# Optimization experiments

Hardware: AMD Instinct MI355X
Metric: run time of the kernel (lower is better)

Reference implementation:

```python
import jax, jax.numpy as jnp
import numpy as np
import math

C = 512
NUM_HEADS = 4
GROUPS = 32  # group_count(512, 32)
EPS = 1e-5


def group_norm(x, gamma, beta):
    # x: [b, c, h, w]; normalize over (c//GROUPS, h, w) per group
    b, c, h, w = x.shape
    xg = x.reshape(b, GROUPS, -1)
    mu = jnp.mean(xg, axis=-1, keepdims=True)
    var = jnp.var(xg, axis=-1, keepdims=True)
    xn = ((xg - mu) * jax.lax.rsqrt(var + EPS)).reshape(b, c, h, w)
    return xn * gamma[None, :, None, None] + beta[None, :, None, None]


def setup_inputs() -> dict:
    key = jax.random.key(0)
    ks = jax.random.split(key, 5)
    b, h, w = 2, 64, 64
    x = jax.random.normal(ks[0], (b, C, h, w), dtype=jnp.float32)
    gn_w = jnp.ones((C,), dtype=jnp.float32)
    gn_b = jnp.zeros((C,), dtype=jnp.float32)
    s_qkv = 1.0 / math.sqrt(C)
    w_qkv = jax.random.uniform(ks[1], (3 * C, C), jnp.float32, -s_qkv, s_qkv)
    b_qkv = jax.random.uniform(ks[2], (3 * C,), jnp.float32, -s_qkv, s_qkv)
    w_proj = jax.random.uniform(ks[3], (C, C), jnp.float32, -s_qkv, s_qkv)
    b_proj = jax.random.uniform(ks[4], (C,), jnp.float32, -s_qkv, s_qkv)
    return {"x": x, "gn_w": gn_w, "gn_b": gn_b, "w_qkv": w_qkv,
            "b_qkv": b_qkv, "w_proj": w_proj, "b_proj": b_proj}


def reference(x, gn_w, gn_b, w_qkv, b_qkv, w_proj, b_proj):
    b, c, h, w = x.shape
    L = h * w
    nh = NUM_HEADS
    hd = c // nh
    residual = x
    xn = group_norm(x, gn_w, gn_b).reshape(b, c, L)
    # Conv1d with kernel_size=1 == channelwise linear: [b, 3c, L]
    qkv = jnp.einsum('bcl,oc->bol', xn, w_qkv) + b_qkv[None, :, None]
    q, k, v = jnp.split(qkv, 3, axis=1)
    q = q.reshape(b, nh, hd, L)
    k = k.reshape(b, nh, hd, L)
    v = v.reshape(b, nh, hd, L)
    scores = jnp.einsum('bncd,bnce->bnde', q, k) / math.sqrt(hd)
    attn = jax.nn.softmax(scores, axis=-1)
    out = jnp.einsum('bnde,bnce->bncd', attn, v).reshape(b, c, L)
    out = jnp.einsum('bcl,oc->bol', out, w_proj) + b_proj[None, :, None]
    return out.reshape(b, c, h, w) + residual
```

## Files before the change

### kernel.cpp

```cpp
#include <hip/hip_runtime.h>
#include <math.h>

typedef __bf16 bf16;
typedef __bf16 bf16x8 __attribute__((ext_vector_type(8)));
typedef __bf16 bf16x4 __attribute__((ext_vector_type(4)));
typedef float f32x4 __attribute__((ext_vector_type(4)));

#define QSCALE (0.08838834764831845f * 1.4426950408889634f)

__device__ __forceinline__ void gll16(const bf16* g, bf16* l) {
    __builtin_amdgcn_global_load_lds((const __attribute__((address_space(1))) void*)g,
                                     (__attribute__((address_space(3))) void*)l, 16, 0, 0);
}

__global__ void k_pre(const float* __restrict__ wqkv, const float* __restrict__ wproj,
                      const float* __restrict__ x,
                      bf16* __restrict__ wqkv_b, bf16* __restrict__ wproj_b,
                      float* __restrict__ part) {
    int blk = blockIdx.x;
    if (blk < 1024) {
        int i = blk * 256 + threadIdx.x;
        const int n1 = (1536 * 512) / 4;
        float4 v;
        bf16* dst;
        if (i < n1) { v = ((const float4*)wqkv)[i];      dst = wqkv_b + (size_t)i * 4; }
        else        { v = ((const float4*)wproj)[i - n1]; dst = wproj_b + (size_t)(i - n1) * 4; }
        bf16x4 o;
        o[0] = (bf16)v.x; o[1] = (bf16)v.y; o[2] = (bf16)v.z; o[3] = (bf16)v.w;
        *(bf16x4*)dst = o;
        return;
    }
    int b2 = blk - 1024;
    int grp = b2 >> 2, p = b2 & 3;
    const float4* src = (const float4*)(x + (size_t)grp * 65536 + (size_t)p * 16384);
    float s = 0.f, ss = 0.f;
    for (int it = 0; it < 16; ++it) {
        float4 v = src[threadIdx.x + it * 256];
        s  += v.x + v.y + v.z + v.w;
        ss += v.x * v.x + v.y * v.y + v.z * v.z + v.w * v.w;
    }
    for (int off = 32; off; off >>= 1) { s += __shfl_down(s, off); ss += __shfl_down(ss, off); }
    __shared__ float rs[4], rss[4];
    int wave = threadIdx.x >> 6;
    if ((threadIdx.x & 63) == 0) { rs[wave] = s; rss[wave] = ss; }
    __syncthreads();
    if (threadIdx.x == 0) {
        part[(grp * 4 + p) * 2]     = rs[0] + rs[1] + rs[2] + rs[3];
        part[(grp * 4 + p) * 2 + 1] = rss[0] + rss[1] + rss[2] + rss[3];
    }
}

__global__ __launch_bounds__(256) void k_gn_norm_t(const float* __restrict__ x, const float* __restrict__ gw,
                                                   const float* __restrict__ gb, const float* __restrict__ part,
                                                   bf16* __restrict__ xn_t) {
    __shared__ float sX[64 * 69];
    __shared__ float sMean[4], sRstd[4];
    int b = blockIdx.z, c0 = blockIdx.y * 64, l0 = blockIdx.x * 64;
    int t = threadIdx.x;
    if (t < 4) {
        int g = b * 32 + (c0 >> 4) + t;
        float S = 0.f, SS = 0.f;
        for (int p = 0; p < 4; ++p) { S += part[(g * 4 + p) * 2]; SS += part[(g * 4 + p) * 2 + 1]; }
        float mean = S * (1.f / 65536.f);
        float var  = SS * (1.f / 65536.f) - mean * mean;
        sMean[t] = mean;
        sRstd[t] = rsqrtf(var + 1e-5f);
    }
    __syncthreads();
    int cr = t >> 4, lq = t & 15;
    const float* xp = x + ((size_t)(b * 512 + c0)) * 4096 + l0;
    for (int i = 0; i < 4; ++i) {
        int c = cr + i * 16;
        int cg = c0 + c;
        float mean = sMean[c >> 4], rstd = sRstd[c >> 4];
        float ga = gw[cg] * rstd;
        float be = gb[cg] - mean * ga;
        float4 v = *(const float4*)(xp + (size_t)c * 4096 + lq * 4);
        float* d = &sX[c * 69 + lq * 4];
        d[0] = v.x * ga + be; d[1] = v.y * ga + be; d[2] = v.z * ga + be; d[3] = v.w * ga + be;
    }
    __syncthreads();
    int lr = t >> 3, cp = t & 7;
    bf16* dst = xn_t + ((size_t)b * 4096 + l0) * 512 + c0;
    for (int i = 0; i < 2; ++i) {
        int l = lr + i * 32;
        bf16x8 o;
        for (int j = 0; j < 8; ++j) o[j] = (bf16)sX[(cp * 8 + j) * 69 + l];
        *(bf16x8*)(dst + (size_t)l * 512 + cp * 8) = o;
    }
}

__global__ __launch_bounds__(256, 3) void k_gemm_qkv(
    const bf16* __restrict__ A, const bf16* __restrict__ W, const float* __restrict__ bias,
    bf16* __restrict__ qkT, bf16* __restrict__ vb) {
    __shared__ bf16 smem[17408];
    int linear = blockIdx.x + 12 * blockIdx.y + 384 * blockIdx.z;
    int swz = (linear & 7) * 96 + (linear >> 3);
    int n0 = (swz % 12) * 128;
    int m0 = ((swz / 12) % 32) * 128;
    int bz = swz / 384;
    int tid = threadIdx.x, lane = tid & 63, wave = tid >> 6;
    int lo = lane & 15, quad = lane >> 4;
    int lr = lane >> 3, ls = lane & 7;
    int mw = (wave >> 1) * 64, nw = (wave & 1) * 64;
    const bf16* aptr[4]; int adst[4];
    const bf16* bptr[4]; int bdst[4];
    for (int i = 0; i < 4; ++i) {
        int r0 = wave * 32 + i * 8;
        int row = r0 + lr;
        aptr[i] = A + (size_t)bz * (4096 * 512) + (size_t)(m0 + row) * 512 + ((ls ^ (row & 7)) * 8);
        adst[i] = r0 * 64;
        bptr[i] = W + (size_t)(n0 + row) * 512 + ((ls ^ (row & 7)) * 8);
        bdst[i] = 8192 + r0 * 64;
    }
    f32x4 acc[4][4] = {};
    for (int step = 0; step < 8; ++step) {
        __syncthreads();
        for (int i = 0; i < 4; ++i) {
            gll16(aptr[i], &smem[adst[i]]); aptr[i] += 64;
            gll16(bptr[i], &smem[bdst[i]]); bptr[i] += 64;
        }
        __syncthreads();
        const bf16* sA = smem;
        const bf16* sB = smem + 8192;
        for (int kk = 0; kk < 2; ++kk) {
            bf16x8 af[4], bfr[4];
            int sw = ((kk * 4 + quad) ^ (lo & 7)) * 8;
            for (int t = 0; t < 4; ++t) af[t]  = *(const bf16x8*)&sA[(mw + t * 16 + lo) * 64 + sw];
            for (int t = 0; t < 4; ++t) bfr[t] = *(const bf16x8*)&sB[(nw + t * 16 + lo) * 64 + sw];
            for (int mt = 0; mt < 4; ++mt)
                for (int nt = 0; nt < 4; ++nt)
                    acc[mt][nt] = __builtin_amdgcn_mfma_f32_16x16x32_bf16(af[mt], bfr[nt], acc[mt][nt], 0, 0, 0);
        }
    }
    __syncthreads();
    bf16* sT = smem;
    bool isv = (n0 >= 1024);
    float sc = (n0 < 512) ? QSCALE : 1.f;
    for (int mt = 0; mt < 4; ++mt)
        for (int nt = 0; nt < 4; ++nt) {
            int c = nw + nt * 16 + lo;
            float bv = bias[n0 + c];
            for (int r = 0; r < 4; ++r) {
                int l = mw + mt * 16 + quad * 4 + r;
                float v = (acc[mt][nt][r] + bv) * sc;
                if (isv) sT[c * 136 + l] = (bf16)v;
                else     sT[l * 136 + c] = (bf16)v;
            }
        }
    __syncthreads();
    int row = tid >> 1, hh = tid & 1;
    if (isv) {
        bf16* dst = vb + (size_t)bz * (512 * 4096) + (size_t)(n0 - 1024 + row) * 4096 + m0;
        for (int j = 0; j < 8; ++j) {
            int ch = hh + j * 2;
            *(bf16x8*)(dst + ch * 8) = *(const bf16x8*)&sT[row * 136 + ch * 8];
        }
    } else {
        bf16* dst = qkT + (size_t)bz * (4096 * 1024) + (size_t)(m0 + row) * 1024 + n0;
        for (int j = 0; j < 8; ++j) {
            int ch = hh + j * 2;
            *(bf16x8*)(dst + ch * 8) = *(const bf16x8*)&sT[row * 136 + ch * 8];
        }
    }
}

__global__ __launch_bounds__(256) void k_gemm_proj(
    const bf16* __restrict__ W, const bf16* __restrict__ Bm,
    const float* __restrict__ bias_m,
    float* __restrict__ outf, const float* __restrict__ resid) {
    constexpr int BUF = (128 + 128) * 64;
    __shared__ bf16 smem[2 * BUF];
    int linear = blockIdx.x + 32 * blockIdx.y + 128 * blockIdx.z;
    int swz = (linear & 7) * 32 + (linear >> 3);
    int n0 = (swz % 32) * 128;
    int m0 = ((swz / 32) % 4) * 128;
    int bz = swz / 128;
    int tid = threadIdx.x, lane = tid & 63, wave = tid >> 6;
    int lo = lane & 15, quad = lane >> 4;
    int lr = lane >> 3, ls = lane & 7;
    int mw = (wave >> 1) * 64, nw = (wave & 1) * 64;
    const bf16* aptr[4]; int adst[4];
    const bf16* bptr[4]; int bdst[4];
    for (int i = 0; i < 4; ++i) {
        int r0 = wave * 32 + i * 8;
        int row = r0 + lr;
        aptr[i] = W + (size_t)(m0 + row) * 512 + ((ls ^ (row & 7)) * 8);
        adst[i] = r0 * 64;
        bptr[i] = Bm + (size_t)bz * (4096 * 512) + (size_t)(n0 + row) * 512 + ((ls ^ (row & 7)) * 8);
        bdst[i] = 8192 + r0 * 64;
    }
    f32x4 acc[4][4] = {};
    for (int i = 0; i < 4; ++i) {
        gll16(aptr[i], &smem[adst[i]]); aptr[i] += 64;
        gll16(bptr[i], &smem[bdst[i]]); bptr[i] += 64;
    }
    for (int step = 0; step < 8; ++step) {
        int cur = step & 1;
        __syncthreads();
        if (step < 7) {
            bf16* nb = &smem[(cur ^ 1) * BUF];
            for (int i = 0; i < 4; ++i) {
                gll16(aptr[i], nb + adst[i]); aptr[i] += 64;
                gll16(bptr[i], nb + bdst[i]); bptr[i] += 64;
            }
        }
        const bf16* sA = &smem[cur * BUF];
        const bf16* sB = sA + 8192;
        for (int kk = 0; kk < 2; ++kk) {
            bf16x8 af[4], bfr[4];
            int sw = ((kk * 4 + quad) ^ (lo & 7)) * 8;
            for (int t = 0; t < 4; ++t) af[t]  = *(const bf16x8*)&sA[(mw + t * 16 + lo) * 64 + sw];
            for (int t = 0; t < 4; ++t) bfr[t] = *(const bf16x8*)&sB[(nw + t * 16 + lo) * 64 + sw];
            for (int mt = 0; mt < 4; ++mt)
                for (int nt = 0; nt < 4; ++nt)
                    acc[mt][nt] = __builtin_amdgcn_mfma_f32_16x16x32_bf16(af[mt], bfr[nt], acc[mt][nt], 0, 0, 0);
        }
    }
    for (int mt = 0; mt < 4; ++mt) {
        int rowb = m0 + mw + mt * 16 + quad * 4;
        for (int nt = 0; nt < 4; ++nt) {
            int col = n0 + nw + nt * 16 + lo;
            for (int r = 0; r < 4; ++r) {
                int row = rowb + r;
                size_t idx = (size_t)bz * (512 * 4096) + (size_t)row * 4096 + col;
                outf[idx] = acc[mt][nt][r] + bias_m[row] + resid[idx];
            }
        }
    }
}

__global__ __launch_bounds__(512, 2) void k_attn(const bf16* __restrict__ qkT, const bf16* __restrict__ vmat,
                                                 bf16* __restrict__ attnT) {
    __shared__ __align__(16) char smem[163840];
    bf16* sE = (bf16*)smem;
    int bidx = blockIdx.x;
    int bh = bidx & 7;
    int bb = bh >> 2, h = bh & 3;
    int l0 = (bidx >> 3) * 128;
    int tid = threadIdx.x, lane = tid & 63, wave = tid >> 6;
    int lo = lane & 15, quad = lane >> 4;
    int a = wave & 3, b2 = wave >> 2;
    const bf16* qbase = qkT + ((size_t)bb * 4096 + l0) * 1024 + h * 128;
    const bf16* kbase = qkT + (size_t)bb * 4096 * 1024 + 512 + h * 128;
    const bf16* vbase = vmat + (size_t)(bb * 512 + h * 128) * 4096;
    for (int i = 0; i < 4; ++i) {
        int r0 = wave * 16 + i * 4;
        int row = r0 + quad;
        gll16(qbase + (size_t)row * 1024 + ((lo ^ (row & 15)) * 8), sE + r0 * 128);
    }
    __syncthreads();
    bf16x8 qf[2][4];
    for (int nt = 0; nt < 2; ++nt) {
        int row = a * 32 + nt * 16 + lo;
        for (int kk = 0; kk < 4; ++kk)
            qf[nt][kk] = *(const bf16x8*)&sE[row * 128 + (((kk * 4 + quad) ^ lo) * 8)];
    }
    __syncthreads();
    const bf16* kp[4]; int kdst[4];
    const bf16* vp[4]; int vdst[4];
    for (int i = 0; i < 4; ++i) {
        int r0 = wave * 16 + i * 4;
        int row = r0 + quad;
        kp[i] = kbase + (size_t)row * 1024 + ((lo ^ (row & 15)) * 8);
        kdst[i] = r0 * 128;
        vp[i] = vbase + (size_t)row * 4096 + ((lo ^ (row & 15)) * 8);
        vdst[i] = 32768 + r0 * 128;
    }
    char* sPb = smem + 131072 + wave * 4096;
    int swz8 = lo & 7;
    float l_r[2];
    l_r[0] = l_r[1] = 0.f;
    f32x4 oacc[8][2] = {};
    for (int i = 0; i < 4; ++i) { gll16(kp[i], sE + kdst[i]); kp[i] += (size_t)128 * 1024; }
    for (int i = 0; i < 4; ++i) { gll16(vp[i], sE + vdst[i]); vp[i] += 128; }
    for (int it = 0; it < 32; ++it) {
        int cur = it & 1;
        __syncthreads();
        if (it < 31) {
            int nb = (cur ^ 1) * 16384;
            for (int i = 0; i < 4; ++i) { gll16(kp[i], sE + nb + kdst[i]); kp[i] += (size_t)128 * 1024; }
            for (int i = 0; i < 4; ++i) { gll16(vp[i], sE + nb + vdst[i]); vp[i] += 128; }
        }
        const bf16* sK = sE + cur * 16384;
        const bf16* sV = sE + 32768 + cur * 16384;
        f32x4 s[4][2];
        __builtin_amdgcn_s_setprio(1);
        for (int mt = 0; mt < 4; ++mt) {
            int krow = b2 * 64 + mt * 16 + lo;
            f32x4 s0 = {}, s1 = {};
            for (int kk = 0; kk < 4; ++kk) {
                bf16x8 kf = *(const bf16x8*)&sK[krow * 128 + (((kk * 4 + quad) ^ lo) * 8)];
                s0 = __builtin_amdgcn_mfma_f32_16x16x32_bf16(kf, qf[0][kk], s0, 0, 0, 0);
                s1 = __builtin_amdgcn_mfma_f32_16x16x32_bf16(kf, qf[1][kk], s1, 0, 0, 0);
            }
            s[mt][0] = s0;
            s[mt][1] = s1;
        }
        __builtin_amdgcn_s_setprio(0);
        for (int mt = 0; mt < 4; ++mt) {
            int cw = (((2 * mt + (quad >> 1)) ^ swz8) << 4) + ((quad & 1) << 3);
            float sm0 = 0.f, sm1 = 0.f;
            bf16x4 pk;
            for (int r = 0; r < 4; ++r) { float pv = __builtin_amdgcn_exp2f(s[mt][0][r]); sm0 += pv; pk[r] = (bf16)pv; }
            *(bf16x4*)&sPb[lo * 128 + cw] = pk;
            for (int r = 0; r < 4; ++r) { float pv = __builtin_amdgcn_exp2f(s[mt][1][r]); sm1 += pv; pk[r] = (bf16)pv; }
            *(bf16x4*)&sPb[(16 + lo) * 128 + cw] = pk;
            l_r[0] += sm0;
            l_r[1] += sm1;
        }
        bf16x8 pf[2][2];
        for (int nt = 0; nt < 2; ++nt)
            for (int kk = 0; kk < 2; ++kk)
                pf[nt][kk] = *(const bf16x8*)&sPb[(nt * 16 + lo) * 128 + (((kk * 4 + quad) ^ swz8) << 4)];
        __builtin_amdgcn_s_setprio(1);
        for (int mt2 = 0; mt2 < 8; ++mt2) {
            int vrow = mt2 * 16 + lo;
            for (int kk = 0; kk < 2; ++kk) {
                bf16x8 vf = *(const bf16x8*)&sV[vrow * 128 + (((b2 * 8 + kk * 4 + quad) ^ lo) * 8)];
                oacc[mt2][0] = __builtin_amdgcn_mfma_f32_16x16x32_bf16(vf, pf[0][kk], oacc[mt2][0], 0, 0, 0);
                oacc[mt2][1] = __builtin_amdgcn_mfma_f32_16x16x32_bf16(vf, pf[1][kk], oacc[mt2][1], 0, 0, 0);
            }
        }
        __builtin_amdgcn_s_setprio(0);
    }
    for (int nt = 0; nt < 2; ++nt) {
        l_r[nt] += __shfl_xor(l_r[nt], 16);
        l_r[nt] += __shfl_xor(l_r[nt], 32);
    }
    __syncthreads();
    float* sStat = (float*)(smem + 139264);
    if (quad == 0) {
        for (int nt = 0; nt < 2; ++nt) {
            int qb = a * 32 + nt * 16 + lo;
            sStat[qb * 2 + b2] = l_r[nt];
        }
    }
    __syncthreads();
    float inv[2];
    for (int nt = 0; nt < 2; ++nt) {
        int qb = a * 32 + nt * 16 + lo;
        inv[nt] = 1.f / (sStat[qb * 2] + sStat[qb * 2 + 1]);
    }
    float* sOm = (float*)smem;
    bf16* sOut = (bf16*)(smem + 67584);
    if (b2 == 1) {
        for (int mt2 = 0; mt2 < 8; ++mt2)
            for (int nt = 0; nt < 2; ++nt)
                for (int r = 0; r < 4; ++r) {
                    int vc = mt2 * 16 + quad * 4 + r;
                    sOm[a * 4224 + vc * 33 + nt * 16 + lo] = oacc[mt2][nt][r];
                }
    }
    __syncthreads();
    if (b2 == 0) {
        for (int mt2 = 0; mt2 < 8; ++mt2)
            for (int nt = 0; nt < 2; ++nt)
                for (int r = 0; r < 4; ++r) {
                    int vc = mt2 * 16 + quad * 4 + r;
                    float v = (oacc[mt2][nt][r] + sOm[a * 4224 + vc * 33 + nt * 16 + lo]) * inv[nt];
                    sOut[(a * 32 + nt * 16 + lo) * 136 + vc] = (bf16)v;
                }
    }
    __syncthreads();
    bf16* dst = attnT + ((size_t)bb * 4096 + l0) * 512 + h * 128;
    for (int i = 0; i < 4; ++i) {
        int row = (tid >> 4) + i * 32;
        int chunk = tid & 15;
        bf16x8 v = *(const bf16x8*)&sOut[row * 136 + chunk * 8];
        *(bf16x8*)(dst + (size_t)row * 512 + chunk * 8) = v;
    }
}

extern "C" void kernel_launch(void* const* d_in, const int* in_sizes, int n_in,
                              void* d_out, int out_size, void* d_ws, size_t ws_size,
                              hipStream_t stream) {
    const float* x      = (const float*)d_in[0];
    const float* gn_w   = (const float*)d_in[1];
    const float* gn_b   = (const float*)d_in[2];
    const float* w_qkv  = (const float*)d_in[3];
    const float* b_qkv  = (const float*)d_in[4];
    const float* w_proj = (const float*)d_in[5];
    const float* b_proj = (const float*)d_in[6];
    float* out = (float*)d_out;
    char* ws = (char*)d_ws;
    bf16* wqkv_b  = (bf16*)(ws + 0);
    bf16* wproj_b = (bf16*)(ws + 1572864);
    bf16* xn_t    = (bf16*)(ws + 2097152);
    bf16* qkT     = (bf16*)(ws + 10485760);
    bf16* vb      = (bf16*)(ws + 27262976);
    bf16* attnT   = (bf16*)(ws + 35651584);
    float* part   = (float*)(ws + 44040192);

    k_pre<<<1280, 256, 0, stream>>>(w_qkv, w_proj, x, wqkv_b, wproj_b, part);
    k_gn_norm_t<<<dim3(64, 8, 2), 256, 0, stream>>>(x, gn_w, gn_b, part, xn_t);
    k_gemm_qkv<<<dim3(12, 32, 2), 256, 0, stream>>>(xn_t, wqkv_b, b_qkv, qkT, vb);
    k_attn<<<256, 512, 0, stream>>>(qkT, vb, attnT);
    k_gemm_proj<<<dim3(32, 4, 2), 256, 0, stream>>>(wproj_b, attnT, b_proj, out, x);
}
```

Baseline: 184.4 us.

## Split attention KV tile into halves to interleave QK, softmax and PV

Each 64-key iteration of the attention loop is split into two 32-key halves. The QK MFMAs for the second half are issued together with the PV MFMAs for the first half, and exp2 for the second half follows, so matrix-core work can overlap the transcendental and LDS work. Register pressure for the score tile drops, at the cost of more sequential phases and extra LDS round-trips for P within the wave.

```diff
diff --git a/kernel.cpp b/kernel.cpp
--- a/kernel.cpp
+++ b/kernel.cpp
@@ -284,9 +284,9 @@
         }
         const bf16* sK = sE + cur * 16384;
         const bf16* sV = sE + 32768 + cur * 16384;
-        f32x4 s[4][2];
+        f32x4 s[2][2];
         __builtin_amdgcn_s_setprio(1);
-        for (int mt = 0; mt < 4; ++mt) {
+        for (int mt = 0; mt < 2; ++mt) {
             int krow = b2 * 64 + mt * 16 + lo;
             f32x4 s0 = {}, s1 = {};
             for (int kk = 0; kk < 4; ++kk) {
@@ -298,7 +298,7 @@
             s[mt][1] = s1;
         }
         __builtin_amdgcn_s_setprio(0);
-        for (int mt = 0; mt < 4; ++mt) {
+        for (int mt = 0; mt < 2; ++mt) {
             int cw = (((2 * mt + (quad >> 1)) ^ swz8) << 4) + ((quad & 1) << 3);
             float sm0 = 0.f, sm1 = 0.f;
             bf16x4 pk;
@@ -309,18 +309,48 @@
             l_r[0] += sm0;
             l_r[1] += sm1;
         }
-        bf16x8 pf[2][2];
+        bf16x8 pf0[2];
         for (int nt = 0; nt < 2; ++nt)
-            for (int kk = 0; kk < 2; ++kk)
-                pf[nt][kk] = *(const bf16x8*)&sPb[(nt * 16 + lo) * 128 + (((kk * 4 + quad) ^ swz8) << 4)];
+            pf0[nt] = *(const bf16x8*)&sPb[(nt * 16 + lo) * 128 + ((quad ^ swz8) << 4)];
+        __builtin_amdgcn_s_setprio(1);
+        for (int mt = 2; mt < 4; ++mt) {
+            int krow = b2 * 64 + mt * 16 + lo;
+            f32x4 s0 = {}, s1 = {};
+            for (int kk = 0; kk < 4; ++kk) {
+                bf16x8 kf = *(const bf16x8*)&sK[krow * 128 + (((kk * 4 + quad) ^ lo) * 8)];
+                s0 = __builtin_amdgcn_mfma_f32_16x16x32_bf16(kf, qf[0][kk], s0, 0, 0, 0);
+                s1 = __builtin_amdgcn_mfma_f32_16x16x32_bf16(kf, qf[1][kk], s1, 0, 0, 0);
+            }
+            s[mt - 2][0] = s0;
+            s[mt - 2][1] = s1;
+        }
+        for (int mt2 = 0; mt2 < 8; ++mt2) {
+            int vrow = mt2 * 16 + lo;
+            bf16x8 vf = *(const bf16x8*)&sV[vrow * 128 + (((b2 * 8 + quad) ^ lo) * 8)];
+            oacc[mt2][0] = __builtin_amdgcn_mfma_f32_16x16x32_bf16(vf, pf0[0], oacc[mt2][0], 0, 0, 0);
+            oacc[mt2][1] = __builtin_amdgcn_mfma_f32_16x16x32_bf16(vf, pf0[1], oacc[mt2][1], 0, 0, 0);
+        }
+        __builtin_amdgcn_s_setprio(0);
+        for (int mt = 2; mt < 4; ++mt) {
+            int cw = (((2 * mt + (quad >> 1)) ^ swz8) << 4) + ((quad & 1) << 3);
+            float sm0 = 0.f, sm1 = 0.f;
+            bf16x4 pk;
+            for (int r = 0; r < 4; ++r) { float pv = __builtin_amdgcn_exp2f(s[mt - 2][0][r]); sm0 += pv; pk[r] = (bf16)pv; }
+            *(bf16x4*)&sPb[lo * 128 + cw] = pk;
+            for (int r = 0; r < 4; ++r) { float pv = __builtin_amdgcn_exp2f(s[mt - 2][1][r]); sm1 += pv; pk[r] = (bf16)pv; }
+            *(bf16x4*)&sPb[(16 + lo) * 128 + cw] = pk;
+            l_r[0] += sm0;
+            l_r[1] += sm1;
+        }
+        bf16x8 pf1[2];
+        for (int nt = 0; nt < 2; ++nt)
+            pf1[nt] = *(const bf16x8*)&sPb[(nt * 16 + lo) * 128 + (((4 + quad) ^ swz8) << 4)];
         __builtin_amdgcn_s_setprio(1);
         for (int mt2 = 0; mt2 < 8; ++mt2) {
             int vrow = mt2 * 16 + lo;
-            for (int kk = 0; kk < 2; ++kk) {
-                bf16x8 vf = *(const bf16x8*)&sV[vrow * 128 + (((b2 * 8 + kk * 4 + quad) ^ lo) * 8)];
-                oacc[mt2][0] = __builtin_amdgcn_mfma_f32_16x16x32_bf16(vf, pf[0][kk], oacc[mt2][0], 0, 0, 0);
-                oacc[mt2][1] = __builtin_amdgcn_mfma_f32_16x16x32_bf16(vf, pf[1][kk], oacc[mt2][1], 0, 0, 0);
-            }
+            bf16x8 vf = *(const bf16x8*)&sV[vrow * 128 + (((b2 * 8 + 4 + quad) ^ lo) * 8)];
+            oacc[mt2][0] = __builtin_amdgcn_mfma_f32_16x16x32_bf16(vf, pf1[0], oacc[mt2][0], 0, 0, 0);
+            oacc[mt2][1] = __builtin_amdgcn_mfma_f32_16x16x32_bf16(vf, pf1[1], oacc[mt2][1], 0, 0, 0);
         }
         __builtin_amdgcn_s_setprio(0);
     }
```

New measurement: 188.7 us. 1.02x slower.
